# Performance work log

Hardware: AMD Instinct MI355X
Metric: run time of the kernel (lower is better)

## Reference

```python
import jax, jax.numpy as jnp
import numpy as np

NUM_USERS = 600000
NUM_ITEMS = 400000
NUM_NODES = NUM_USERS + NUM_ITEMS
DIM = 64
NUM_EDGES = 8000000


def setup_inputs() -> dict:
    key = jax.random.key(0)
    k1, k2, k3, k4 = jax.random.split(key, 4)
    users_emb = jax.random.normal(k1, (NUM_USERS, DIM), dtype=jnp.float32)
    items_emb = jax.random.normal(k2, (NUM_ITEMS, DIM), dtype=jnp.float32)
    edge_index = jax.random.randint(k3, (2, NUM_EDGES), 0, NUM_NODES, dtype=jnp.int64)
    edge_values = jax.random.uniform(k4, (NUM_EDGES,), dtype=jnp.float32)
    return {
        "users_emb": users_emb,
        "items_emb": items_emb,
        "edge_index": edge_index,
        "edge_values": edge_values,
    }


def reference(users_emb, items_emb, edge_index, edge_values):
    # all_emb = cat([users_emb, items_emb])  -> [N, d]
    num_user = users_emb.shape[0]
    num_item = items_emb.shape[0]
    all_emb = jnp.concatenate([users_emb, items_emb], axis=0)
    # SpMM: out[r] = sum_{e: row[e]==r} val[e] * all_emb[col[e]]
    rows, cols = edge_index[0], edge_index[1]
    messages = all_emb[cols] * edge_values[:, None]  # [E, d] gather + scale
    out = jax.ops.segment_sum(messages, rows, num_segments=num_user + num_item)
    h_u2 = out[:num_user]
    h_i2 = out[num_user:]
    return (h_u2, h_i2)
```

## Files before the change

### kernel.cpp

```cpp
#include <hip/hip_runtime.h>

#define DIM 64
#define RPB 1024
#define RPB_SHIFT 10
#define NBMAX 1024
#define CHUNK 4096
#define EPT 16
#define CAPT 35
#define SREC_CAP (CAPT * 256)
#define NPGF 32

typedef unsigned long long u64;
typedef unsigned int u32;
typedef unsigned short u16;
typedef float f4v __attribute__((ext_vector_type(4)));
typedef _Float16 h4 __attribute__((ext_vector_type(4)));
typedef _Float16 h8 __attribute__((ext_vector_type(8)));

__global__ void detect_idx_width(const unsigned int* __restrict__ idx_words,
                                 int* __restrict__ flag,
                                 int* __restrict__ counts) {
    __shared__ unsigned int s_or[256];
    if (counts)
        for (int i = threadIdx.x; i < NBMAX; i += 256) counts[i] = 0;
    unsigned int acc = 0;
    for (int i = threadIdx.x; i < 4096; i += blockDim.x)
        acc |= idx_words[2 * i + 1];
    s_or[threadIdx.x] = acc;
    __syncthreads();
    for (int s = 128; s > 0; s >>= 1) {
        if (threadIdx.x < s) s_or[threadIdx.x] |= s_or[threadIdx.x + s];
        __syncthreads();
    }
    if (threadIdx.x == 0) *flag = (s_or[0] == 0) ? 1 : 0;
}

__device__ __forceinline__ int load_idx(const void* ei, int use64, long long i) {
    return use64 ? (int)((const long long*)ei)[i] : ((const int*)ei)[i];
}

__device__ __forceinline__ int load_idx_nt(const void* ei, int use64, long long i) {
    return use64 ? (int)__builtin_nontemporal_load(&((const long long*)ei)[i])
                 : __builtin_nontemporal_load(&((const int*)ei)[i]);
}

__device__ __forceinline__ u32 quad_scan_ex(u32 qs, u32* wtot, int tid, u32* total_out) {
    u32 inc = qs;
    #pragma unroll
    for (int d = 1; d < 64; d <<= 1) {
        u32 v = __shfl_up(inc, d, 64);
        if ((tid & 63) >= d) inc += v;
    }
    if ((tid & 63) == 63) wtot[tid >> 6] = inc;
    __syncthreads();
    int w = tid >> 6;
    u32 woff = 0;
    #pragma unroll
    for (int k = 0; k < 3; ++k) woff += (k < w) ? wtot[k] : 0;
    if (total_out) *total_out = wtot[0] + wtot[1] + wtot[2] + wtot[3];
    return woff + inc - qs;
}

__global__ __launch_bounds__(256) void prep(const f4v* __restrict__ u4,
                                            const f4v* __restrict__ i4,
                                            long long usz4, long long tot4,
                                            h4* __restrict__ dst,
                                            const void* __restrict__ ei,
                                            const int* __restrict__ flag,
                                            int* __restrict__ counts,
                                            int num_edges,
                                            int convBlocks, int histBlocks) {
    if ((int)blockIdx.x < convBlocks) {
        long long stride = (long long)convBlocks * 256;
        for (long long idx = (long long)blockIdx.x * 256 + threadIdx.x;
             idx < tot4; idx += stride) {
            const f4v* src = (idx < usz4) ? (u4 + idx) : (i4 + (idx - usz4));
            f4v f = __builtin_nontemporal_load(src);
            h4 o;
            o.x = (_Float16)f.x; o.y = (_Float16)f.y;
            o.z = (_Float16)f.z; o.w = (_Float16)f.w;
            dst[idx] = o;
        }
    } else {
        __shared__ int h[NBMAX];
        for (int b = threadIdx.x; b < NBMAX; b += 256) h[b] = 0;
        __syncthreads();
        int use64 = *flag;
        int hb = (int)blockIdx.x - convBlocks;
        long long tid = (long long)hb * 256 + threadIdx.x;
        long long stride = (long long)histBlocks * 256;
        long long npairs = (long long)num_edges >> 1;
        const u64* p = (const u64*)ei;
        if (use64) {
            for (long long e = tid; e < npairs; e += stride) {
                u64 a = __builtin_nontemporal_load(&p[2 * e]);
                u64 b = __builtin_nontemporal_load(&p[2 * e + 1]);
                atomicAdd(&h[(int)(u32)a >> RPB_SHIFT], 1);
                atomicAdd(&h[(int)(u32)b >> RPB_SHIFT], 1);
            }
        } else {
            for (long long e = tid; e < npairs; e += stride) {
                u64 v = __builtin_nontemporal_load(&p[e]);
                atomicAdd(&h[(int)(u32)v >> RPB_SHIFT], 1);
                atomicAdd(&h[(int)(u32)(v >> 32) >> RPB_SHIFT], 1);
            }
        }
        if (tid == 0 && (num_edges & 1)) {
            int r = load_idx(ei, use64, num_edges - 1);
            atomicAdd(&h[r >> RPB_SHIFT], 1);
        }
        __syncthreads();
        for (int b = threadIdx.x; b < NBMAX; b += 256)
            if (h[b]) atomicAdd(&counts[b], h[b]);
    }
}

__global__ __launch_bounds__(256) void hist_coarse(const void* __restrict__ ei,
                                                   const int* __restrict__ flag,
                                                   int* __restrict__ counts,
                                                   int num_edges) {
    __shared__ int h[NBMAX];
    for (int b = threadIdx.x; b < NBMAX; b += 256) h[b] = 0;
    __syncthreads();
    int use64 = *flag;
    long long tid = (long long)blockIdx.x * 256 + threadIdx.x;
    long long stride = (long long)gridDim.x * 256;
    long long npairs = (long long)num_edges >> 1;
    const u64* p = (const u64*)ei;
    if (use64) {
        for (long long e = tid; e < npairs; e += stride) {
            u64 a = __builtin_nontemporal_load(&p[2 * e]);
            u64 b = __builtin_nontemporal_load(&p[2 * e + 1]);
            atomicAdd(&h[(int)(u32)a >> RPB_SHIFT], 1);
            atomicAdd(&h[(int)(u32)b >> RPB_SHIFT], 1);
        }
    } else {
        for (long long e = tid; e < npairs; e += stride) {
            u64 v = __builtin_nontemporal_load(&p[e]);
            atomicAdd(&h[(int)(u32)v >> RPB_SHIFT], 1);
            atomicAdd(&h[(int)(u32)(v >> 32) >> RPB_SHIFT], 1);
        }
    }
    if (tid == 0 && (num_edges & 1)) {
        int r = load_idx(ei, use64, num_edges - 1);
        atomicAdd(&h[r >> RPB_SHIFT], 1);
    }
    __syncthreads();
    for (int b = threadIdx.x; b < NBMAX; b += 256)
        if (h[b]) atomicAdd(&counts[b], h[b]);
}

__global__ __launch_bounds__(256) void scan_buckets(const int* __restrict__ counts,
                                                    int* __restrict__ offs,
                                                    int* __restrict__ gcursor,
                                                    int* __restrict__ offs2, int nbkt) {
    __shared__ u32 wtot[4];
    int t = threadIdx.x;
    int4 h = ((const int4*)counts)[t];
    u32 qs = (u32)(h.x + h.y + h.z + h.w);
    u32 total;
    u32 ex = quad_scan_ex(qs, wtot, t, &total);
    int o0 = (int)ex, o1 = o0 + h.x, o2 = o1 + h.y, o3 = o2 + h.z;
    offs[4*t] = o0; offs[4*t+1] = o1; offs[4*t+2] = o2; offs[4*t+3] = o3;
    gcursor[4*t] = o0; gcursor[4*t+1] = o1; gcursor[4*t+2] = o2; gcursor[4*t+3] = o3;
    if (t == 255) {
        offs[NBMAX] = (int)total;
        if (offs2) offs2[(long long)nbkt << RPB_SHIFT] = (int)total;
    }
}

__global__ __launch_bounds__(256) void bin_edges(const void* __restrict__ ei,
                                                 const float* __restrict__ vals,
                                                 const int* __restrict__ flag,
                                                 int* __restrict__ gcursor,
                                                 u64* __restrict__ recs,
                                                 int num_edges) {
    __shared__ u32 hist[NBMAX];
    __shared__ u32 scanL[NBMAX];
    __shared__ u32 gbase[NBMAX];
    __shared__ u32 wtot[4];
    __shared__ u64 payload[CHUNK];
    __shared__ u16 bidv[CHUNK];

    int tid = threadIdx.x;
    long long base = (long long)blockIdx.x * CHUNK;
    int n = (int)min((long long)CHUNK, (long long)num_edges - base);
    int use64 = *flag;

    for (int b = tid; b < NBMAX; b += 256) hist[b] = 0;
    __syncthreads();

    int rows_[EPT]; int cols_[EPT]; float ws_[EPT];
    #pragma unroll
    for (int i = 0; i < EPT; ++i) {
        int j = tid + i * 256;
        rows_[i] = -1;
        if (j < n) {
            long long e = base + j;
            rows_[i] = load_idx_nt(ei, use64, e);
            cols_[i] = load_idx_nt(ei, use64, (long long)num_edges + e);
            ws_[i]   = __builtin_nontemporal_load(&vals[e]);
            atomicAdd(&hist[rows_[i] >> RPB_SHIFT], 1u);
        }
    }
    __syncthreads();

    u32 h0 = hist[4*tid], h1 = hist[4*tid+1], h2 = hist[4*tid+2], h3 = hist[4*tid+3];
    u32 ex = quad_scan_ex(h0 + h1 + h2 + h3, wtot, tid, nullptr);
    scanL[4*tid]   = ex;
    scanL[4*tid+1] = ex + h0;
    scanL[4*tid+2] = ex + h0 + h1;
    scanL[4*tid+3] = ex + h0 + h1 + h2;
    __syncthreads();

    for (int b = tid; b < NBMAX; b += 256) {
        u32 c = hist[b];
        gbase[b] = c ? (u32)atomicAdd(&gcursor[b], (int)c) : 0u;
    }
    __syncthreads();
    for (int b = tid; b < NBMAX; b += 256) hist[b] = scanL[b];
    __syncthreads();

    #pragma unroll
    for (int i = 0; i < EPT; ++i) {
        if (rows_[i] >= 0) {
            int b = rows_[i] >> RPB_SHIFT;
            u32 pos = atomicAdd(&hist[b], 1u);
            u32 rl = (u32)(rows_[i] & (RPB - 1));
            payload[pos] = ((u64)__float_as_uint(ws_[i]) << 32) | (rl << 20) | (u32)cols_[i];
            bidv[pos] = (u16)b;
        }
    }
    __syncthreads();

    for (int j = tid; j < n; j += 256) {
        u64 rec = payload[j];
        int b = bidv[j];
        recs[gbase[b] + (u32)j - scanL[b]] = rec;
    }
}

#define ACC8(P0, P1, W, V) \
    P0.x += W * (float)V[0]; P0.y += W * (float)V[1]; \
    P0.z += W * (float)V[2]; P0.w += W * (float)V[3]; \
    P1.x += W * (float)V[4]; P1.y += W * (float)V[5]; \
    P1.z += W * (float)V[6]; P1.w += W * (float)V[7];

__global__ __launch_bounds__(256, 2) void sortgather_h(const int* __restrict__ offs,
                                                       const u64* __restrict__ recs,
                                                       const h8* __restrict__ hemb8,
                                                       float* __restrict__ out,
                                                       int num_nodes) {
    __shared__ u64 s_recs[SREC_CAP];
    __shared__ u32 node_beg[RPB + 1];
    __shared__ u32 cursor[RPB];
    __shared__ u32 wtot[4];

    int b  = blockIdx.x;
    int t  = threadIdx.x;
    int l8 = t & 7;
    int g  = t >> 3;
    int beg = offs[b], end = offs[b + 1];
    int cnt = end - beg;
    int row0 = b << RPB_SHIFT;

    if (cnt <= SREC_CAP) {
        u64 r_[CAPT];
        #pragma unroll
        for (int k = 0; k < CAPT; ++k) {
            int j = t + k * 256;
            r_[k] = (j < cnt) ? __builtin_nontemporal_load(&recs[beg + j]) : 0ull;
        }
        for (int i = t; i < RPB; i += 256) cursor[i] = 0;
        __syncthreads();
        #pragma unroll
        for (int k = 0; k < CAPT; ++k) {
            int j = t + k * 256;
            if (j < cnt) atomicAdd(&cursor[(u32)(r_[k] >> 20) & (RPB - 1)], 1u);
        }
        __syncthreads();
        u32 c0[4]; u32 s = 0;
        #pragma unroll
        for (int i = 0; i < 4; ++i) { c0[i] = cursor[t * 4 + i]; s += c0[i]; }
        u32 ex = quad_scan_ex(s, wtot, t, nullptr);
        #pragma unroll
        for (int i = 0; i < 4; ++i) {
            node_beg[t * 4 + i] = ex;
            cursor[t * 4 + i] = ex;
            ex += c0[i];
        }
        if (t == 0) node_beg[RPB] = (u32)cnt;
        __syncthreads();
        #pragma unroll
        for (int k = 0; k < CAPT; ++k) {
            int j = t + k * 256;
            if (j < cnt) {
                u32 rl = (u32)(r_[k] >> 20) & (RPB - 1);
                u32 pos = atomicAdd(&cursor[rl], 1u);
                s_recs[pos] = r_[k];
            }
        }
        __syncthreads();

        for (int nn = 0; nn < NPGF; ++nn) {
            int ln = g * NPGF + nn;
            int node = row0 + ln;
            if (node >= num_nodes) break;
            int nb = (int)node_beg[ln];
            int ne = (int)node_beg[ln + 1];

            float4 p0 = make_float4(0.f,0.f,0.f,0.f), p1 = make_float4(0.f,0.f,0.f,0.f);
            float4 q0 = make_float4(0.f,0.f,0.f,0.f), q1 = make_float4(0.f,0.f,0.f,0.f);

            int i = nb;
            for (; i + 8 <= ne; i += 8) {
                u64 s0 = s_recs[i];     u64 s1 = s_recs[i + 1];
                u64 s2 = s_recs[i + 2]; u64 s3 = s_recs[i + 3];
                u64 s4 = s_recs[i + 4]; u64 s5 = s_recs[i + 5];
                u64 s6 = s_recs[i + 6]; u64 s7 = s_recs[i + 7];
                h8 v0 = hemb8[(((u32)s0 & 0xFFFFFu) << 3) + l8];
                h8 v1 = hemb8[(((u32)s1 & 0xFFFFFu) << 3) + l8];
                h8 v2 = hemb8[(((u32)s2 & 0xFFFFFu) << 3) + l8];
                h8 v3 = hemb8[(((u32)s3 & 0xFFFFFu) << 3) + l8];
                h8 v4 = hemb8[(((u32)s4 & 0xFFFFFu) << 3) + l8];
                h8 v5 = hemb8[(((u32)s5 & 0xFFFFFu) << 3) + l8];
                h8 v6 = hemb8[(((u32)s6 & 0xFFFFFu) << 3) + l8];
                h8 v7 = hemb8[(((u32)s7 & 0xFFFFFu) << 3) + l8];
                float w0 = __uint_as_float((u32)(s0 >> 32));
                float w1 = __uint_as_float((u32)(s1 >> 32));
                float w2 = __uint_as_float((u32)(s2 >> 32));
                float w3 = __uint_as_float((u32)(s3 >> 32));
                float w4 = __uint_as_float((u32)(s4 >> 32));
                float w5 = __uint_as_float((u32)(s5 >> 32));
                float w6 = __uint_as_float((u32)(s6 >> 32));
                float w7 = __uint_as_float((u32)(s7 >> 32));
                ACC8(p0, p1, w0, v0); ACC8(q0, q1, w1, v1);
                ACC8(p0, p1, w2, v2); ACC8(q0, q1, w3, v3);
                ACC8(p0, p1, w4, v4); ACC8(q0, q1, w5, v5);
                ACC8(p0, p1, w6, v6); ACC8(q0, q1, w7, v7);
            }
            if (i < ne) {
                int last = ne - 1;
                int e1 = min(i + 1, last), e2 = min(i + 2, last);
                int e3 = min(i + 3, last), e4 = min(i + 4, last);
                int e5 = min(i + 5, last), e6 = min(i + 6, last);
                u64 s0 = s_recs[i];  u64 s1 = s_recs[e1];
                u64 s2 = s_recs[e2]; u64 s3 = s_recs[e3];
                u64 s4 = s_recs[e4]; u64 s5 = s_recs[e5];
                u64 s6 = s_recs[e6];
                h8 v0 = hemb8[(((u32)s0 & 0xFFFFFu) << 3) + l8];
                h8 v1 = hemb8[(((u32)s1 & 0xFFFFFu) << 3) + l8];
                h8 v2 = hemb8[(((u32)s2 & 0xFFFFFu) << 3) + l8];
                h8 v3 = hemb8[(((u32)s3 & 0xFFFFFu) << 3) + l8];
                h8 v4 = hemb8[(((u32)s4 & 0xFFFFFu) << 3) + l8];
                h8 v5 = hemb8[(((u32)s5 & 0xFFFFFu) << 3) + l8];
                h8 v6 = hemb8[(((u32)s6 & 0xFFFFFu) << 3) + l8];
                float w0 = __uint_as_float((u32)(s0 >> 32));
                float w1 = (i + 1 < ne) ? __uint_as_float((u32)(s1 >> 32)) : 0.f;
                float w2 = (i + 2 < ne) ? __uint_as_float((u32)(s2 >> 32)) : 0.f;
                float w3 = (i + 3 < ne) ? __uint_as_float((u32)(s3 >> 32)) : 0.f;
                float w4 = (i + 4 < ne) ? __uint_as_float((u32)(s4 >> 32)) : 0.f;
                float w5 = (i + 5 < ne) ? __uint_as_float((u32)(s5 >> 32)) : 0.f;
                float w6 = (i + 6 < ne) ? __uint_as_float((u32)(s6 >> 32)) : 0.f;
                ACC8(p0, p1, w0, v0); ACC8(q0, q1, w1, v1);
                ACC8(p0, p1, w2, v2); ACC8(q0, q1, w3, v3);
                ACC8(p0, p1, w4, v4); ACC8(q0, q1, w5, v5);
                ACC8(p0, p1, w6, v6);
            }

            p0.x += q0.x; p0.y += q0.y; p0.z += q0.z; p0.w += q0.w;
            p1.x += q1.x; p1.y += q1.y; p1.z += q1.z; p1.w += q1.w;
            f4v o0; o0.x = p0.x; o0.y = p0.y; o0.z = p0.z; o0.w = p0.w;
            f4v o1; o1.x = p1.x; o1.y = p1.y; o1.z = p1.z; o1.w = p1.w;
            f4v* dst = (f4v*)out + ((long long)node << 4) + (l8 << 1);
            __builtin_nontemporal_store(o0, dst);
            __builtin_nontemporal_store(o1, dst + 1);
        }
    } else {
        for (int nn = 0; nn < NPGF; ++nn) {
            int ln = g * NPGF + nn;
            int node = row0 + ln;
            if (node >= num_nodes) break;
            u32 rl = (u32)ln;

            float4 p0 = make_float4(0.f,0.f,0.f,0.f), p1 = make_float4(0.f,0.f,0.f,0.f);
            float4 q0 = make_float4(0.f,0.f,0.f,0.f), q1 = make_float4(0.f,0.f,0.f,0.f);
            int last = end - 1;
            u32 rm = RPB - 1;
            for (int i = beg; i < end; i += 4) {
                int e1 = min(i + 1, last), e2 = min(i + 2, last), e3 = min(i + 3, last);
                u64 s0 = recs[i];  u64 s1 = recs[e1];
                u64 s2 = recs[e2]; u64 s3 = recs[e3];
                h8 v0 = hemb8[(((u32)s0 & 0xFFFFFu) << 3) + l8];
                h8 v1 = hemb8[(((u32)s1 & 0xFFFFFu) << 3) + l8];
                h8 v2 = hemb8[(((u32)s2 & 0xFFFFFu) << 3) + l8];
                h8 v3 = hemb8[(((u32)s3 & 0xFFFFFu) << 3) + l8];
                float w0 = ((((u32)(s0 >> 20)) & rm) == rl)
                           ? __uint_as_float((u32)(s0 >> 32)) : 0.f;
                float w1 = (((((u32)(s1 >> 20)) & rm) == rl) & (i + 1 < end))
                           ? __uint_as_float((u32)(s1 >> 32)) : 0.f;
                float w2 = (((((u32)(s2 >> 20)) & rm) == rl) & (i + 2 < end))
                           ? __uint_as_float((u32)(s2 >> 32)) : 0.f;
                float w3 = (((((u32)(s3 >> 20)) & rm) == rl) & (i + 3 < end))
                           ? __uint_as_float((u32)(s3 >> 32)) : 0.f;
                ACC8(p0, p1, w0, v0); ACC8(q0, q1, w1, v1);
                ACC8(p0, p1, w2, v2); ACC8(q0, q1, w3, v3);
            }
            p0.x += q0.x; p0.y += q0.y; p0.z += q0.z; p0.w += q0.w;
            p1.x += q1.x; p1.y += q1.y; p1.z += q1.z; p1.w += q1.w;
            f4v o0; o0.x = p0.x; o0.y = p0.y; o0.z = p0.z; o0.w = p0.w;
            f4v o1; o1.x = p1.x; o1.y = p1.y; o1.z = p1.z; o1.w = p1.w;
            f4v* dst = (f4v*)out + ((long long)node << 4) + (l8 << 1);
            __builtin_nontemporal_store(o0, dst);
            __builtin_nontemporal_store(o1, dst + 1);
        }
    }
}

__global__ __launch_bounds__(256, 2) void sort_bucket(const int* __restrict__ offs,
                                                      u64* __restrict__ recs,
                                                      int* __restrict__ offs2) {
    __shared__ u32 bins[RPB];
    __shared__ u32 wtot[4];
    int b = blockIdx.x;
    int t = threadIdx.x;
    int beg = offs[b], end = offs[b + 1];
    int cnt = end - beg;
    int row0 = b << RPB_SHIFT;

    if (cnt > CAPT * 256) {
        for (int i = t; i < RPB; i += 256) offs2[row0 + i] = -(b + 1);
        return;
    }

    u64 r_[CAPT];
    #pragma unroll
    for (int k = 0; k < CAPT; ++k) {
        int j = t + k * 256;
        r_[k] = (j < cnt) ? recs[beg + j] : 0ull;
    }
    for (int i = t; i < RPB; i += 256) bins[i] = 0;
    __syncthreads();

    #pragma unroll
    for (int k = 0; k < CAPT; ++k) {
        int j = t + k * 256;
        if (j < cnt) atomicAdd(&bins[(u32)(r_[k] >> 20) & (RPB - 1)], 1u);
    }
    __syncthreads();

    u32 c0[4]; u32 s = 0;
    #pragma unroll
    for (int i = 0; i < 4; ++i) { c0[i] = bins[t * 4 + i]; s += c0[i]; }
    u32 ex = quad_scan_ex(s, wtot, t, nullptr);
    #pragma unroll
    for (int i = 0; i < 4; ++i) {
        bins[t * 4 + i] = ex;
        offs2[row0 + t * 4 + i] = beg + (int)ex;
        ex += c0[i];
    }
    __syncthreads();

    #pragma unroll
    for (int k = 0; k < CAPT; ++k) {
        int j = t + k * 256;
        if (j < cnt) {
            u32 rl = (u32)(r_[k] >> 20) & (RPB - 1);
            u32 pos = atomicAdd(&bins[rl], 1u);
            recs[beg + pos] = r_[k];
        }
    }
}

__device__ __forceinline__ void gstep(u64 s, u32 rl,
                                      const float* __restrict__ users,
                                      const float* __restrict__ items_m,
                                      int num_users, int l16, float4& a) {
    int c = (int)(s & 0xFFFFFu);
    float w = __uint_as_float((u32)(s >> 32));
    w = (((u32)(s >> 20) & (RPB - 1)) == rl) ? w : 0.f;
    const float* p = ((c < num_users) ? users : items_m) + ((u32)c << 6);
    float4 m = reinterpret_cast<const float4*>(p)[l16];
    a.x += w * m.x; a.y += w * m.y; a.z += w * m.z; a.w += w * m.w;
}

__global__ __launch_bounds__(256) void gather_nodes(const int* __restrict__ offs,
                                                    const int* __restrict__ offs2,
                                                    const u64* __restrict__ recs,
                                                    const float* __restrict__ users,
                                                    const float* __restrict__ items_m,
                                                    float* __restrict__ out,
                                                    int num_users, int num_nodes) {
    int node = blockIdx.x * (blockDim.x >> 6) + (threadIdx.x >> 6);
    int lane = threadIdx.x & 63;
    if (node >= num_nodes) return;
    int q   = lane >> 4;
    int l16 = lane & 15;

    int beg = offs2[node];
    int end = offs2[node + 1];
    if (beg < 0) { int b = node >> RPB_SHIFT; beg = offs[b]; end = offs[b + 1]; }
    else if (end < 0) { end = offs[(node >> RPB_SHIFT) + 1]; }
    u32 rl = (u32)(node & (RPB - 1));

    float4 a0 = make_float4(0.f, 0.f, 0.f, 0.f);
    float4 a1 = make_float4(0.f, 0.f, 0.f, 0.f);

    int i = beg + q;
    for (; i + 4 < end; i += 8) {
        u64 s0 = recs[i];
        u64 s1 = recs[i + 4];
        gstep(s0, rl, users, items_m, num_users, l16, a0);
        gstep(s1, rl, users, items_m, num_users, l16, a1);
    }
    if (i < end) {
        u64 s0 = recs[i];
        gstep(s0, rl, users, items_m, num_users, l16, a0);
    }
    a0.x += a1.x; a0.y += a1.y; a0.z += a1.z; a0.w += a1.w;

    for (int msk = 16; msk <= 32; msk <<= 1) {
        a0.x += __shfl_xor(a0.x, msk, 64);
        a0.y += __shfl_xor(a0.y, msk, 64);
        a0.z += __shfl_xor(a0.z, msk, 64);
        a0.w += __shfl_xor(a0.w, msk, 64);
    }
    if (q == 0)
        reinterpret_cast<float4*>(out)[(long long)node * 16 + l16] = a0;
}

__global__ __launch_bounds__(256) void scatter_edges(const void* __restrict__ edge_index,
                                                     const float* __restrict__ vals,
                                                     const float* __restrict__ users,
                                                     const float* __restrict__ items,
                                                     float* __restrict__ out,
                                                     const int* __restrict__ idx64_flag,
                                                     int num_users, int num_edges) {
    long long gid = (long long)blockIdx.x * blockDim.x + threadIdx.x;
    long long e = gid >> 4;
    int lane = (int)(gid & 15);
    if (e >= num_edges) return;
    int use64 = *idx64_flag;
    int r = load_idx(edge_index, use64, e);
    int c = load_idx(edge_index, use64, (long long)num_edges + e);
    float w = vals[e];
    const float* src = (c < num_users)
        ? (users + (long long)c * DIM)
        : (items + (long long)(c - num_users) * DIM);
    float4 m = reinterpret_cast<const float4*>(src)[lane];
    float* dst = out + (long long)r * DIM + lane * 4;
    unsafeAtomicAdd(dst + 0, m.x * w);
    unsafeAtomicAdd(dst + 1, m.y * w);
    unsafeAtomicAdd(dst + 2, m.z * w);
    unsafeAtomicAdd(dst + 3, m.w * w);
}

extern "C" void kernel_launch(void* const* d_in, const int* in_sizes, int n_in,
                              void* d_out, int out_size, void* d_ws, size_t ws_size,
                              hipStream_t stream) {
    const float* users = (const float*)d_in[0];
    const float* items = (const float*)d_in[1];
    const void*  eidx  = d_in[2];
    const float* vals  = (const float*)d_in[3];
    float* out = (float*)d_out;

    int num_users = in_sizes[0] / DIM;
    int num_items = in_sizes[1] / DIM;
    int num_nodes = num_users + num_items;
    int num_edges = in_sizes[3];
    int nbkt = (num_nodes + RPB - 1) >> RPB_SHIFT;

    size_t off = 0;
    auto alloc = [&](size_t bytes) { size_t p = off; off = (off + bytes + 255) & ~(size_t)255; return p; };
    size_t o_flag   = alloc(4);
    size_t o_counts = alloc((size_t)NBMAX * 4);
    size_t o_offs   = alloc(((size_t)NBMAX + 1) * 4);
    size_t o_gcur   = alloc((size_t)NBMAX * 4);
    size_t o_recs   = alloc((size_t)num_edges * 8 + 64);
    size_t o_offs2  = alloc((((size_t)nbkt << RPB_SHIFT) + 1) * 4);
    size_t need_base = off;
    size_t o_hemb   = alloc((size_t)num_nodes * DIM * 2);
    size_t need_f16 = off;

    char* ws = (char*)d_ws;
    int* flag = (int*)(ws + o_flag);

    if (ws_size < need_base || nbkt > NBMAX || num_nodes > (1 << 20)) {
        detect_idx_width<<<1, 256, 0, stream>>>((const unsigned int*)eidx, flag, nullptr);
        hipMemsetAsync(d_out, 0, (size_t)out_size * sizeof(float), stream);
        long long total_threads = (long long)num_edges * 16;
        long long grid = (total_threads + 255) / 256;
        scatter_edges<<<(int)grid, 256, 0, stream>>>(
            eidx, vals, users, items, out, flag, num_users, num_edges);
        return;
    }

    int* counts  = (int*)(ws + o_counts);
    int* offs    = (int*)(ws + o_offs);
    int* gcursor = (int*)(ws + o_gcur);
    u64* recs    = (u64*)(ws + o_recs);
    int* offs2   = (int*)(ws + o_offs2);
    h4*  hemb4   = (h4*)(ws + o_hemb);

    bool use_f16 = (ws_size >= need_f16) && ((DIM % 8) == 0);

    detect_idx_width<<<1, 256, 0, stream>>>((const unsigned int*)eidx, flag, counts);

    long long usz4 = (long long)num_users * DIM / 4;
    long long tot4 = (long long)num_nodes * DIM / 4;

    if (use_f16) {
        const int convB = 2048, histB = 768;
        prep<<<convB + histB, 256, 0, stream>>>((const f4v*)users, (const f4v*)items,
                                                usz4, tot4, hemb4,
                                                eidx, flag, counts, num_edges,
                                                convB, histB);
    } else {
        hist_coarse<<<768, 256, 0, stream>>>(eidx, flag, counts, num_edges);
    }

    scan_buckets<<<1, 256, 0, stream>>>(counts, offs, gcursor,
                                        use_f16 ? nullptr : offs2, nbkt);

    int bin_grid = (num_edges + CHUNK - 1) / CHUNK;
    bin_edges<<<bin_grid, 256, 0, stream>>>(eidx, vals, flag, gcursor, recs, num_edges);

    if (use_f16) {
        sortgather_h<<<nbkt, 256, 0, stream>>>(offs, recs, (const h8*)hemb4,
                                               out, num_nodes);
    } else {
        sort_bucket<<<nbkt, 256, 0, stream>>>(offs, recs, offs2);
        int gg = (num_nodes + 3) / 4;
        const float* items_m = items - (size_t)num_users * DIM;
        gather_nodes<<<gg, 256, 0, stream>>>(offs, offs2, recs, users, items_m, out,
                                             num_users, num_nodes);
    }
}
```

Before: 386.9 us.

## Split gather into two half-row phases with 4 lanes per node

The fast path of the sorted gather now assigns 4 lanes per node instead of 8 and makes two passes, each gathering one 64-byte half of the fp16 embedding row. Each group handles 16 nodes per pass, so twice as many nodes are in flight across the block. The likely intent is to cut the number of distinct cache lines touched at once, or to improve locality within each phase. In exchange, the shared-memory record reads and loop overhead are doubled, and each row is fetched as two separate half-line accesses.

```diff
diff --git a/kernel.cpp b/kernel.cpp
--- a/kernel.cpp
+++ b/kernel.cpp
@@ -8,7 +8,7 @@
 #define EPT 16
 #define CAPT 35
 #define SREC_CAP (CAPT * 256)
-#define NPGF 32
+#define NPG4 16
 
 typedef unsigned long long u64;
 typedef unsigned int u32;
@@ -258,8 +258,6 @@
 
     int b  = blockIdx.x;
     int t  = threadIdx.x;
-    int l8 = t & 7;
-    int g  = t >> 3;
     int beg = offs[b], end = offs[b + 1];
     int cnt = end - beg;
     int row0 = b << RPB_SHIFT;
@@ -302,83 +300,90 @@
         }
         __syncthreads();
 
-        for (int nn = 0; nn < NPGF; ++nn) {
-            int ln = g * NPGF + nn;
-            int node = row0 + ln;
-            if (node >= num_nodes) break;
-            int nb = (int)node_beg[ln];
-            int ne = (int)node_beg[ln + 1];
-
-            float4 p0 = make_float4(0.f,0.f,0.f,0.f), p1 = make_float4(0.f,0.f,0.f,0.f);
-            float4 q0 = make_float4(0.f,0.f,0.f,0.f), q1 = make_float4(0.f,0.f,0.f,0.f);
-
-            int i = nb;
-            for (; i + 8 <= ne; i += 8) {
-                u64 s0 = s_recs[i];     u64 s1 = s_recs[i + 1];
-                u64 s2 = s_recs[i + 2]; u64 s3 = s_recs[i + 3];
-                u64 s4 = s_recs[i + 4]; u64 s5 = s_recs[i + 5];
-                u64 s6 = s_recs[i + 6]; u64 s7 = s_recs[i + 7];
-                h8 v0 = hemb8[(((u32)s0 & 0xFFFFFu) << 3) + l8];
-                h8 v1 = hemb8[(((u32)s1 & 0xFFFFFu) << 3) + l8];
-                h8 v2 = hemb8[(((u32)s2 & 0xFFFFFu) << 3) + l8];
-                h8 v3 = hemb8[(((u32)s3 & 0xFFFFFu) << 3) + l8];
-                h8 v4 = hemb8[(((u32)s4 & 0xFFFFFu) << 3) + l8];
-                h8 v5 = hemb8[(((u32)s5 & 0xFFFFFu) << 3) + l8];
-                h8 v6 = hemb8[(((u32)s6 & 0xFFFFFu) << 3) + l8];
-                h8 v7 = hemb8[(((u32)s7 & 0xFFFFFu) << 3) + l8];
-                float w0 = __uint_as_float((u32)(s0 >> 32));
-                float w1 = __uint_as_float((u32)(s1 >> 32));
-                float w2 = __uint_as_float((u32)(s2 >> 32));
-                float w3 = __uint_as_float((u32)(s3 >> 32));
-                float w4 = __uint_as_float((u32)(s4 >> 32));
-                float w5 = __uint_as_float((u32)(s5 >> 32));
-                float w6 = __uint_as_float((u32)(s6 >> 32));
-                float w7 = __uint_as_float((u32)(s7 >> 32));
-                ACC8(p0, p1, w0, v0); ACC8(q0, q1, w1, v1);
-                ACC8(p0, p1, w2, v2); ACC8(q0, q1, w3, v3);
-                ACC8(p0, p1, w4, v4); ACC8(q0, q1, w5, v5);
-                ACC8(p0, p1, w6, v6); ACC8(q0, q1, w7, v7);
+        int l4 = t & 3;
+        int g4 = t >> 2;
+        for (int ph = 0; ph < 2; ++ph) {
+            const h8* tab = hemb8 + (ph << 2) + l4;
+            for (int nn = 0; nn < NPG4; ++nn) {
+                int ln = g4 * NPG4 + nn;
+                int node = row0 + ln;
+                if (node >= num_nodes) break;
+                int nb = (int)node_beg[ln];
+                int ne = (int)node_beg[ln + 1];
+
+                float4 p0 = make_float4(0.f,0.f,0.f,0.f), p1 = make_float4(0.f,0.f,0.f,0.f);
+                float4 q0 = make_float4(0.f,0.f,0.f,0.f), q1 = make_float4(0.f,0.f,0.f,0.f);
+
+                int i = nb;
+                for (; i + 8 <= ne; i += 8) {
+                    u64 s0 = s_recs[i];     u64 s1 = s_recs[i + 1];
+                    u64 s2 = s_recs[i + 2]; u64 s3 = s_recs[i + 3];
+                    u64 s4 = s_recs[i + 4]; u64 s5 = s_recs[i + 5];
+                    u64 s6 = s_recs[i + 6]; u64 s7 = s_recs[i + 7];
+                    h8 v0 = tab[((u32)s0 & 0xFFFFFu) << 3];
+                    h8 v1 = tab[((u32)s1 & 0xFFFFFu) << 3];
+                    h8 v2 = tab[((u32)s2 & 0xFFFFFu) << 3];
+                    h8 v3 = tab[((u32)s3 & 0xFFFFFu) << 3];
+                    h8 v4 = tab[((u32)s4 & 0xFFFFFu) << 3];
+                    h8 v5 = tab[((u32)s5 & 0xFFFFFu) << 3];
+                    h8 v6 = tab[((u32)s6 & 0xFFFFFu) << 3];
+                    h8 v7 = tab[((u32)s7 & 0xFFFFFu) << 3];
+                    float w0 = __uint_as_float((u32)(s0 >> 32));
+                    float w1 = __uint_as_float((u32)(s1 >> 32));
+                    float w2 = __uint_as_float((u32)(s2 >> 32));
+                    float w3 = __uint_as_float((u32)(s3 >> 32));
+                    float w4 = __uint_as_float((u32)(s4 >> 32));
+                    float w5 = __uint_as_float((u32)(s5 >> 32));
+                    float w6 = __uint_as_float((u32)(s6 >> 32));
+                    float w7 = __uint_as_float((u32)(s7 >> 32));
+                    ACC8(p0, p1, w0, v0); ACC8(q0, q1, w1, v1);
+                    ACC8(p0, p1, w2, v2); ACC8(q0, q1, w3, v3);
+                    ACC8(p0, p1, w4, v4); ACC8(q0, q1, w5, v5);
+                    ACC8(p0, p1, w6, v6); ACC8(q0, q1, w7, v7);
+                }
+                if (i < ne) {
+                    int last = ne - 1;
+                    int e1 = min(i + 1, last), e2 = min(i + 2, last);
+                    int e3 = min(i + 3, last), e4 = min(i + 4, last);
+                    int e5 = min(i + 5, last), e6 = min(i + 6, last);
+                    u64 s0 = s_recs[i];  u64 s1 = s_recs[e1];
+                    u64 s2 = s_recs[e2]; u64 s3 = s_recs[e3];
+                    u64 s4 = s_recs[e4]; u64 s5 = s_recs[e5];
+                    u64 s6 = s_recs[e6];
+                    h8 v0 = tab[((u32)s0 & 0xFFFFFu) << 3];
+                    h8 v1 = tab[((u32)s1 & 0xFFFFFu) << 3];
+                    h8 v2 = tab[((u32)s2 & 0xFFFFFu) << 3];
+                    h8 v3 = tab[((u32)s3 & 0xFFFFFu) << 3];
+                    h8 v4 = tab[((u32)s4 & 0xFFFFFu) << 3];
+                    h8 v5 = tab[((u32)s5 & 0xFFFFFu) << 3];
+                    h8 v6 = tab[((u32)s6 & 0xFFFFFu) << 3];
+                    float w0 = __uint_as_float((u32)(s0 >> 32));
+                    float w1 = (i + 1 < ne) ? __uint_as_float((u32)(s1 >> 32)) : 0.f;
+                    float w2 = (i + 2 < ne) ? __uint_as_float((u32)(s2 >> 32)) : 0.f;
+                    float w3 = (i + 3 < ne) ? __uint_as_float((u32)(s3 >> 32)) : 0.f;
+                    float w4 = (i + 4 < ne) ? __uint_as_float((u32)(s4 >> 32)) : 0.f;
+                    float w5 = (i + 5 < ne) ? __uint_as_float((u32)(s5 >> 32)) : 0.f;
+                    float w6 = (i + 6 < ne) ? __uint_as_float((u32)(s6 >> 32)) : 0.f;
+                    ACC8(p0, p1, w0, v0); ACC8(q0, q1, w1, v1);
+                    ACC8(p0, p1, w2, v2); ACC8(q0, q1, w3, v3);
+                    ACC8(p0, p1, w4, v4); ACC8(q0, q1, w5, v5);
+                    ACC8(p0, p1, w6, v6);
+                }
+
+                p0.x += q0.x; p0.y += q0.y; p0.z += q0.z; p0.w += q0.w;
+                p1.x += q1.x; p1.y += q1.y; p1.z += q1.z; p1.w += q1.w;
+                f4v o0; o0.x = p0.x; o0.y = p0.y; o0.z = p0.z; o0.w = p0.w;
+                f4v o1; o1.x = p1.x; o1.y = p1.y; o1.z = p1.z; o1.w = p1.w;
+                f4v* dst = (f4v*)out + ((long long)node << 4) + (ph << 3) + (l4 << 1);
+                __builtin_nontemporal_store(o0, dst);
+                __builtin_nontemporal_store(o1, dst + 1);
             }
-            if (i < ne) {
-                int last = ne - 1;
-                int e1 = min(i + 1, last), e2 = min(i + 2, last);
-                int e3 = min(i + 3, last), e4 = min(i + 4, last);
-                int e5 = min(i + 5, last), e6 = min(i + 6, last);
-                u64 s0 = s_recs[i];  u64 s1 = s_recs[e1];
-                u64 s2 = s_recs[e2]; u64 s3 = s_recs[e3];
-                u64 s4 = s_recs[e4]; u64 s5 = s_recs[e5];
-                u64 s6 = s_recs[e6];
-                h8 v0 = hemb8[(((u32)s0 & 0xFFFFFu) << 3) + l8];
-                h8 v1 = hemb8[(((u32)s1 & 0xFFFFFu) << 3) + l8];
-                h8 v2 = hemb8[(((u32)s2 & 0xFFFFFu) << 3) + l8];
-                h8 v3 = hemb8[(((u32)s3 & 0xFFFFFu) << 3) + l8];
-                h8 v4 = hemb8[(((u32)s4 & 0xFFFFFu) << 3) + l8];
-                h8 v5 = hemb8[(((u32)s5 & 0xFFFFFu) << 3) + l8];
-                h8 v6 = hemb8[(((u32)s6 & 0xFFFFFu) << 3) + l8];
-                float w0 = __uint_as_float((u32)(s0 >> 32));
-                float w1 = (i + 1 < ne) ? __uint_as_float((u32)(s1 >> 32)) : 0.f;
-                float w2 = (i + 2 < ne) ? __uint_as_float((u32)(s2 >> 32)) : 0.f;
-                float w3 = (i + 3 < ne) ? __uint_as_float((u32)(s3 >> 32)) : 0.f;
-                float w4 = (i + 4 < ne) ? __uint_as_float((u32)(s4 >> 32)) : 0.f;
-                float w5 = (i + 5 < ne) ? __uint_as_float((u32)(s5 >> 32)) : 0.f;
-                float w6 = (i + 6 < ne) ? __uint_as_float((u32)(s6 >> 32)) : 0.f;
-                ACC8(p0, p1, w0, v0); ACC8(q0, q1, w1, v1);
-                ACC8(p0, p1, w2, v2); ACC8(q0, q1, w3, v3);
-                ACC8(p0, p1, w4, v4); ACC8(q0, q1, w5, v5);
-                ACC8(p0, p1, w6, v6);
-            }
-
-            p0.x += q0.x; p0.y += q0.y; p0.z += q0.z; p0.w += q0.w;
-            p1.x += q1.x; p1.y += q1.y; p1.z += q1.z; p1.w += q1.w;
-            f4v o0; o0.x = p0.x; o0.y = p0.y; o0.z = p0.z; o0.w = p0.w;
-            f4v o1; o1.x = p1.x; o1.y = p1.y; o1.z = p1.z; o1.w = p1.w;
-            f4v* dst = (f4v*)out + ((long long)node << 4) + (l8 << 1);
-            __builtin_nontemporal_store(o0, dst);
-            __builtin_nontemporal_store(o1, dst + 1);
         }
     } else {
-        for (int nn = 0; nn < NPGF; ++nn) {
-            int ln = g * NPGF + nn;
+        int l8 = t & 7;
+        int g8 = t >> 3;
+        for (int nn = 0; nn < 32; ++nn) {
+            int ln = g8 * 32 + nn;
             int node = row0 + ln;
             if (node >= num_nodes) break;
             u32 rl = (u32)ln;
```

New measurement: 530.2 us. 1.37x slower.
